# Performance work log

Measured on AMD Instinct MI355X. Metric: run time of the kernel, lower is better.

Reference implementation:

```python
import jax, jax.numpy as jnp
import numpy as np

N_EDGES = 8192
TOTAL_TOKENS = 2097152
OUT_CH = 128


def setup_inputs() -> dict:
    key = jax.random.key(0)
    k1, k2, k3, k4, k5 = jax.random.split(key, 5)
    overlap_similarity = jax.random.uniform(k1, (N_EDGES,), dtype=jnp.float32)
    overlap_length = jax.random.normal(k2, (N_EDGES,), dtype=jnp.float32)
    # flattened DNA tokens (A,C,G,T -> 0..3) over all edges
    tokens = jax.random.randint(k3, (TOTAL_TOKENS,), 0, 4, dtype=jnp.int32)
    # sorted segment ids -> ragged variable-length reads per edge
    segment_ids = jnp.sort(jax.random.randint(k4, (TOTAL_TOKENS,), 0, N_EDGES, dtype=jnp.int32))
    embedding = jax.random.normal(k5, (4, OUT_CH), dtype=jnp.float32)
    return {
        "overlap_similarity": overlap_similarity,
        "overlap_length": overlap_length,
        "tokens": tokens,
        "segment_ids": segment_ids,
        "embedding": embedding,
        "n_edges": N_EDGES,
    }


def reference(overlap_similarity, overlap_length, tokens, segment_ids, embedding, n_edges):
    # Ragged embedding-bag mean: for each edge, mean of embedding[tokens] over its read.
    # (overlap_similarity / overlap_length are unused by the original forward's output.)
    embeds = embedding[tokens]  # [T, D]
    sums = jax.ops.segment_sum(embeds, segment_ids, num_segments=n_edges)  # [E, D]
    counts = jax.ops.segment_sum(
        jnp.ones((tokens.shape[0],), dtype=embeds.dtype), segment_ids, num_segments=n_edges
    )  # [E]
    return sums / jnp.maximum(counts, 1.0)[:, None]
```

## Files before the change

kernel.cpp:

```cpp
#include <hip/hip_runtime.h>

#define OUT_CH 128
#define WAVES_PER_BLOCK 4

__global__ __launch_bounds__(WAVES_PER_BLOCK * 64)
void edge_fused_kernel(const int* __restrict__ tokens,
                       const int* __restrict__ segids,
                       const float* __restrict__ emb,
                       float* __restrict__ out,
                       int T, int E) {
    const int lane = threadIdx.x & 63;
    const int wid  = threadIdx.x >> 6;
    const int e = blockIdx.x * WAVES_PER_BLOCK + wid;
    if (e >= E) return;

    int lo0 = 0, hi0 = T;
    int lo1 = 0, hi1 = T;
    while ((lo0 < hi0) | (lo1 < hi1)) {
        int mid0 = (lo0 + hi0) >> 1;
        int mid1 = (lo1 + hi1) >> 1;
        int v0 = (lo0 < hi0) ? segids[mid0] : 0x7FFFFFFF;
        int v1 = (lo1 < hi1) ? segids[mid1] : 0x7FFFFFFF;
        if (lo0 < hi0) { if (v0 < e)     lo0 = mid0 + 1; else hi0 = mid0; }
        if (lo1 < hi1) { if (v1 < e + 1) lo1 = mid1 + 1; else hi1 = mid1; }
    }
    const int start = lo0, end = lo1;

    unsigned long long acc = 0;
    for (int k = start + lane; k < end; k += 64) {
        acc += 1ull << (tokens[k] << 4);
    }
    #pragma unroll
    for (int m = 32; m > 0; m >>= 1) {
        acc += __shfl_xor(acc, m, 64);
    }

    const float c0 = (float)(acc & 0xFFFFull);
    const float c1 = (float)((acc >> 16) & 0xFFFFull);
    const float c2 = (float)((acc >> 32) & 0xFFFFull);
    const float c3 = (float)((acc >> 48) & 0xFFFFull);
    const float tot = c0 + c1 + c2 + c3;
    const float inv = 1.0f / fmaxf(tot, 1.0f);

    const int c = lane << 1;
    const float2 e0 = *(const float2*)(emb + 0 * OUT_CH + c);
    const float2 e1 = *(const float2*)(emb + 1 * OUT_CH + c);
    const float2 e2 = *(const float2*)(emb + 2 * OUT_CH + c);
    const float2 e3 = *(const float2*)(emb + 3 * OUT_CH + c);

    float2 r;
    r.x = (c0 * e0.x + c1 * e1.x + c2 * e2.x + c3 * e3.x) * inv;
    r.y = (c0 * e0.y + c1 * e1.y + c2 * e2.y + c3 * e3.y) * inv;
    *(float2*)(out + (size_t)e * OUT_CH + c) = r;
}

extern "C" void kernel_launch(void* const* d_in, const int* in_sizes, int n_in,
                              void* d_out, int out_size, void* d_ws, size_t ws_size,
                              hipStream_t stream) {
    const int* tokens = (const int*)d_in[2];
    const int* segids = (const int*)d_in[3];
    const float* emb  = (const float*)d_in[4];
    float* out = (float*)d_out;

    const int T = in_sizes[2];
    const int E = out_size / OUT_CH;

    const int blocks = (E + WAVES_PER_BLOCK - 1) / WAVES_PER_BLOCK;
    edge_fused_kernel<<<blocks, WAVES_PER_BLOCK * 64, 0, stream>>>(
        tokens, segids, emb, out, T, E);
}
```

Measured before the change: 91.90 us.

## Replace per-edge binary search with a boundary-detection pass building segment start offsets

Adds a first kernel that reads the sorted segment ids in int4 chunks and writes the start offset of each segment wherever adjacent ids differ. The main kernel then reads its start and end from this offsets array instead of running two dependent binary searches over two million entries. This removes about 21 rounds of serially dependent global loads per wave, at the cost of a second launch and an extra full streaming read of the segment ids. It assumes T is a multiple of four for the vector load and that the workspace holds E+1 ints.

```diff
diff --git a/kernel.cpp b/kernel.cpp
--- a/kernel.cpp
+++ b/kernel.cpp
@@ -3,34 +3,43 @@
 #define OUT_CH 128
 #define WAVES_PER_BLOCK 4
 
+__global__ void seg_starts_kernel(const int* __restrict__ segids,
+                                  int* __restrict__ starts,
+                                  int T, int E) {
+    int i = blockIdx.x * blockDim.x + threadIdx.x;
+    int k = i << 2;
+    if (k >= T) return;
+    const int4 s4 = *(const int4*)(segids + k);
+    int s[5] = {s4.x, s4.y, s4.z, s4.w, 0};
+    s[4] = (k + 4 < T) ? segids[k + 4] : E;
+    if (k == 0) {
+        for (int q = 0; q <= s4.x; ++q) starts[q] = 0;
+    }
+#pragma unroll
+    for (int j = 0; j < 4; ++j) {
+        for (int q = s[j] + 1; q <= s[j + 1]; ++q) starts[q] = k + j + 1;
+    }
+}
+
 __global__ __launch_bounds__(WAVES_PER_BLOCK * 64)
-void edge_fused_kernel(const int* __restrict__ tokens,
-                       const int* __restrict__ segids,
-                       const float* __restrict__ emb,
-                       float* __restrict__ out,
-                       int T, int E) {
+void edge_out_kernel(const int* __restrict__ tokens,
+                     const int* __restrict__ starts,
+                     const float* __restrict__ emb,
+                     float* __restrict__ out,
+                     int E) {
     const int lane = threadIdx.x & 63;
     const int wid  = threadIdx.x >> 6;
     const int e = blockIdx.x * WAVES_PER_BLOCK + wid;
     if (e >= E) return;
 
-    int lo0 = 0, hi0 = T;
-    int lo1 = 0, hi1 = T;
-    while ((lo0 < hi0) | (lo1 < hi1)) {
-        int mid0 = (lo0 + hi0) >> 1;
-        int mid1 = (lo1 + hi1) >> 1;
-        int v0 = (lo0 < hi0) ? segids[mid0] : 0x7FFFFFFF;
-        int v1 = (lo1 < hi1) ? segids[mid1] : 0x7FFFFFFF;
-        if (lo0 < hi0) { if (v0 < e)     lo0 = mid0 + 1; else hi0 = mid0; }
-        if (lo1 < hi1) { if (v1 < e + 1) lo1 = mid1 + 1; else hi1 = mid1; }
-    }
-    const int start = lo0, end = lo1;
+    const int start = starts[e];
+    const int end   = starts[e + 1];
 
     unsigned long long acc = 0;
     for (int k = start + lane; k < end; k += 64) {
         acc += 1ull << (tokens[k] << 4);
     }
-    #pragma unroll
+#pragma unroll
     for (int m = 32; m > 0; m >>= 1) {
         acc += __shfl_xor(acc, m, 64);
     }
@@ -65,7 +74,13 @@
     const int T = in_sizes[2];
     const int E = out_size / OUT_CH;
 
-    const int blocks = (E + WAVES_PER_BLOCK - 1) / WAVES_PER_BLOCK;
-    edge_fused_kernel<<<blocks, WAVES_PER_BLOCK * 64, 0, stream>>>(
-        tokens, segids, emb, out, T, E);
+    int* starts = (int*)d_ws;
+
+    const int threadsA = (T + 3) / 4;
+    const int blocksA = (threadsA + 255) / 256;
+    seg_starts_kernel<<<blocksA, 256, 0, stream>>>(segids, starts, T, E);
+
+    const int blocksB = (E + WAVES_PER_BLOCK - 1) / WAVES_PER_BLOCK;
+    edge_out_kernel<<<blocksB, WAVES_PER_BLOCK * 64, 0, stream>>>(
+        tokens, starts, emb, out, E);
 }
```

New measurement: 82.61 us. 10.1% less time.
